# Kernel tuning notes

Measured on AMD Instinct MI355X. Metric: run time of the kernel, lower is better.

The kernel has to match this reference:

```python
import jax, jax.numpy as jnp
import numpy as np

IN_FF = 7  # joints
MASK = np.ones(9, dtype=np.float32)  # [P(3), RPY sin/cos (6)]


def _mlp(x, params):
    # params: list of (W, b); sigmoid after every layer except the last (predict)
    h = x
    for W, b in params[:-1]:
        h = jax.nn.sigmoid(h @ W + b)
    W, b = params[-1]
    return h @ W + b


def _rpy_head(x, params):
    # FeedForwardNet_RPY forward: y -> [sin(y0), cos(y1)], angle = atan2(sin, cos)
    y = _mlp(x, params)
    s = jnp.sin(y[..., 0])
    c = jnp.cos(y[..., 1])
    ang = jnp.arctan2(s, c)
    return jnp.stack([s, c, ang], axis=-1)  # (..., 3)


def setup_inputs():
    key = jax.random.key(0)
    ks = jax.random.split(key, 26)
    m = 16384
    d = {"x": jax.random.normal(ks[0], (m, 2 * IN_FF), jnp.float32)}

    def lin(k, fi, fo, name, i):
        k1, k2 = jax.random.split(k)
        lim = 1.0 / np.sqrt(fi)  # torch Linear default init
        d[name + "_W" + str(i)] = jax.random.uniform(k1, (fi, fo), jnp.float32, -lim, lim)
        d[name + "_b" + str(i)] = jax.random.uniform(k2, (fo,), jnp.float32, -lim, lim)

    idx = 1
    for name, dims in [("pos", [7, 512, 512, 3]), ("roll", [7, 256, 256, 2]),
                       ("pitch", [7, 256, 256, 2]), ("yaw", [7, 256, 256, 2])]:
        for i in range(3):
            lin(ks[idx], dims[i], dims[i + 1], name, i)
            idx += 1
    return d


def _forward(x, pos_p, roll_p, pitch_p, yaw_p):
    mask = jnp.asarray(MASK)
    M_P, M_RPY = mask[:3], mask[3:]
    q, qdot = x[:, :IN_FF], x[:, IN_FF:]

    # position net: forward + per-sample Jacobian (exact, replaces the autograd loop)
    P = _mlp(q, pos_p)                                          # (m, 3)
    J_P = jax.vmap(jax.jacfwd(lambda z: _mlp(z, pos_p)))(q)     # (m, 3, 7)
    vel = jnp.einsum("moi,mi->mo", J_P, qdot)                   # bmm(J_P, jointVels)
    P = P * M_P
    vel = vel * M_P

    heads = []
    for p in (roll_p, pitch_p, yaw_p):
        f = lambda z, p=p: _rpy_head(z, p)
        y = f(q)                                # (m, 3): [sin, cos, angle]
        J = jax.vmap(jax.jacfwd(f))(q)          # (m, 3, 7)
        v = jnp.einsum("moi,mi->mo", J[:, :2, :], qdot)  # (m, 2)
        heads.append((y, J, v))
    (yR, JR, vR), (yPi, JPi, vPi), (yY, JY, vY) = heads

    # order: [roll_sin, pitch_sin, yaw_sin, roll_cos, pitch_cos, yaw_cos]
    RPY = jnp.stack([yR[:, 0], yPi[:, 0], yY[:, 0], yR[:, 1], yPi[:, 1], yY[:, 1]], axis=1) * M_RPY
    vel_RPY = jnp.stack([vR[:, 0], vPi[:, 0], vY[:, 0], vR[:, 1], vPi[:, 1], vY[:, 1]], axis=1) * M_RPY
    J_RPY = jnp.stack([JR[:, 0], JPi[:, 0], JY[:, 0], JR[:, 1], JPi[:, 1], JY[:, 1]], axis=1)  # (m,6,7)

    out = jnp.concatenate([P, RPY, vel, vel_RPY], axis=1)            # (m, 18)
    J_tot = jnp.concatenate([J_P, J_RPY], axis=1)                    # (m, 9, 7)
    out_angles = jnp.concatenate([P, yR[:, 2:3], yPi[:, 2:3], yY[:, 2:3]], axis=1)       # (m, 6)
    J_tot_angles = jnp.concatenate([J_P, JR[:, 2:3], JPi[:, 2:3], JY[:, 2:3]], axis=1)   # (m, 6, 7)
    return out, J_tot, out_angles, J_tot_angles


def reference(x, pos_W0, pos_b0, pos_W1, pos_b1, pos_W2, pos_b2,
              roll_W0, roll_b0, roll_W1, roll_b1, roll_W2, roll_b2,
              pitch_W0, pitch_b0, pitch_W1, pitch_b1, pitch_W2, pitch_b2,
              yaw_W0, yaw_b0, yaw_W1, yaw_b1, yaw_W2, yaw_b2):
    pos_p = [(pos_W0, pos_b0), (pos_W1, pos_b1), (pos_W2, pos_b2)]
    roll_p = [(roll_W0, roll_b0), (roll_W1, roll_b1), (roll_W2, roll_b2)]
    pitch_p = [(pitch_W0, pitch_b0), (pitch_W1, pitch_b1), (pitch_W2, pitch_b2)]
    yaw_p = [(yaw_W0, yaw_b0), (yaw_W1, yaw_b1), (yaw_W2, yaw_b2)]
    return _forward(x, pos_p, roll_p, pitch_p, yaw_p)
```

## Files before the change

### kernel.cpp

```cpp
#include <hip/hip_runtime.h>
#include <math.h>

typedef __attribute__((ext_vector_type(8))) short short8;
typedef __attribute__((ext_vector_type(4))) float floatx4;
typedef __attribute__((ext_vector_type(2))) unsigned uint2v;

__device__ __forceinline__ float sig(float z) { return 1.0f / (1.0f + __expf(-z)); }

__device__ __forceinline__ unsigned short f2bf(float f) {
    unsigned u = __float_as_uint(f);
    u = (u + 0x7FFFu + ((u >> 16) & 1u)) >> 16;
    return (unsigned short)u;
}

__device__ __forceinline__ unsigned cvtpk_bf16(float lo, float hi) {
    unsigned r;
    asm("v_cvt_pk_bf16_f32 %0, %1, %2" : "=v"(r) : "v"(lo), "v"(hi));
    return r;
}

__device__ __forceinline__ void st_pack4(unsigned short* p, float v0, float v1, float v2, float v3) {
    uint2v u;
    u.x = cvtpk_bf16(v0, v1);
    u.y = cvtpk_bf16(v2, v3);
    *(uint2v*)p = u;
}

__global__ void convert_all(const float* __restrict__ s0, const float* __restrict__ s1,
                            const float* __restrict__ s2, const float* __restrict__ s3,
                            unsigned short* __restrict__ ws) {
    int idx = blockIdx.x * 256 + threadIdx.x;
    const float* src; unsigned short* dst; int H, logH, local;
    if (idx < 262144) { src = s0; dst = ws; H = 512; logH = 9; local = idx; }
    else {
        int r = idx - 262144; int m = r >> 16; local = r & 65535;
        H = 256; logH = 8;
        src = (m == 0) ? s1 : (m == 1) ? s2 : s3;
        dst = ws + 262144 + m * 65536;
    }
    int n = local & (H - 1), k = local >> logH;
    int KT = H >> 5;
    int blk = (n >> 4) * KT + (k >> 5);
    int lane = ((k >> 3) & 3) * 16 + (n & 15);
    int j = k & 7;
    dst[(blk * 64 + lane) * 8 + j] = f2bf(src[local]);
}

struct PosS {
    float B0[512], B1[512], W2[1536];
    float Q[4][8], Qd[4][8];
    float Sum[32][3];
};
struct RpyS {
    float B0[256], B1[256], W2[512];
    float Q[8][8], Qd[8][8];
    float Sum[64][2];
};

__global__ __launch_bounds__(256, 3)
void fused_mfma(const float* __restrict__ x,
                const float* __restrict__ pW0, const float* __restrict__ pb0,
                const float* __restrict__ pb1,
                const float* __restrict__ pW2, const float* __restrict__ pb2,
                const float* __restrict__ rW0_, const float* __restrict__ rb0_,
                const float* __restrict__ rb1_,
                const float* __restrict__ rW2_, const float* __restrict__ rb2_,
                const float* __restrict__ piW0, const float* __restrict__ pib0,
                const float* __restrict__ pib1,
                const float* __restrict__ piW2, const float* __restrict__ pib2,
                const float* __restrict__ yW0, const float* __restrict__ yb0,
                const float* __restrict__ yb1,
                const float* __restrict__ yW2, const float* __restrict__ yb2,
                const unsigned short* __restrict__ wsBase,
                float* __restrict__ out, int ns)
{
    extern __shared__ unsigned short sA[];
    __shared__ union { PosS p; RpyS r; } sU;

    const int tid = threadIdx.x;
    const int xcd  = blockIdx.x & 7;
    const int slot = blockIdx.x >> 3;
    const int o_l  = slot / 5, r5 = slot % 5;
    const int o = xcd + (o_l << 3);

    const size_t JTOT = (size_t)ns * 18, OUTA = (size_t)ns * 81, JANG = (size_t)ns * 87;
    const floatx4 z4 = {0.f, 0.f, 0.f, 0.f};
    const int w = tid >> 6, lane = tid & 63;
    const int quad = lane >> 4, col = lane & 15;
    const int srcl = lane & 47;
    const int lxk = lane ^ (quad << 1);

    if (r5 < 2) {
        const int m0 = (o * 2 + r5) * 4;
        const unsigned short* wsW1 = wsBase;

        for (int i = tid; i < 512;  i += 256) { sU.p.B0[i] = pb0[i]; sU.p.B1[i] = pb1[i]; }
        for (int i = tid; i < 1536; i += 256) sU.p.W2[i] = pW2[i];
        if (tid < 56) {
            int m = tid / 14, c = tid % 14;
            float v = x[(m0 + m) * 14 + c];
            if (c < 7) sU.p.Q[m][c] = v; else sU.p.Qd[m][c - 7] = v;
        }
        __syncthreads();

        const float4* W04 = (const float4*)pW0;

        floatx4 acc[2][8];
        #pragma unroll
        for (int rt = 0; rt < 2; rt++)
            #pragma unroll
            for (int ct = 0; ct < 8; ct++) acc[rt][ct] = z4;

        const short8* bbase = (const short8*)wsW1 + (size_t)(w * 8 * 16) * 64 + lane;
        short8 b0[4], b1[4], b2[4];

#define PLD(B, KT) { \
            B[0] = bbase[((cp4 + 0) * 16 + hh8 + (KT)) * 64]; \
            B[1] = bbase[((cp4 + 1) * 16 + hh8 + (KT)) * 64]; \
            B[2] = bbase[((cp4 + 2) * 16 + hh8 + (KT)) * 64]; \
            B[3] = bbase[((cp4 + 3) * 16 + hh8 + (KT)) * 64]; }
#define PST(B, KT) { \
            const short8 a0 = *(const short8*)&sA[(0 * 8 + (KT)) * 512 + (lxk ^ (KT)) * 8]; \
            const short8 a1 = *(const short8*)&sA[(1 * 8 + (KT)) * 512 + (lxk ^ (KT)) * 8]; \
            acc[0][cp4 + 0] = __builtin_amdgcn_mfma_f32_16x16x32_bf16(a0, B[0], acc[0][cp4 + 0], 0, 0, 0); \
            acc[1][cp4 + 0] = __builtin_amdgcn_mfma_f32_16x16x32_bf16(a1, B[0], acc[1][cp4 + 0], 0, 0, 0); \
            acc[0][cp4 + 1] = __builtin_amdgcn_mfma_f32_16x16x32_bf16(a0, B[1], acc[0][cp4 + 1], 0, 0, 0); \
            acc[1][cp4 + 1] = __builtin_amdgcn_mfma_f32_16x16x32_bf16(a1, B[1], acc[1][cp4 + 1], 0, 0, 0); \
            acc[0][cp4 + 2] = __builtin_amdgcn_mfma_f32_16x16x32_bf16(a0, B[2], acc[0][cp4 + 2], 0, 0, 0); \
            acc[1][cp4 + 2] = __builtin_amdgcn_mfma_f32_16x16x32_bf16(a1, B[2], acc[1][cp4 + 2], 0, 0, 0); \
            acc[0][cp4 + 3] = __builtin_amdgcn_mfma_f32_16x16x32_bf16(a0, B[3], acc[0][cp4 + 3], 0, 0, 0); \
            acc[1][cp4 + 3] = __builtin_amdgcn_mfma_f32_16x16x32_bf16(a1, B[3], acc[1][cp4 + 3], 0, 0, 0); }

        #pragma unroll
        for (int hh = 0; hh < 2; ++hh) {
            const int hh8 = hh * 8;
            b0[0] = bbase[(0 * 16 + hh8) * 64];
            b0[1] = bbase[(1 * 16 + hh8) * 64];
            b0[2] = bbase[(2 * 16 + hh8) * 64];
            b0[3] = bbase[(3 * 16 + hh8) * 64];
            {
                const int jh = tid & 1, item = tid >> 1;
                const int s = item >> 5, k8l = item & 31, k8 = (hh << 5) | k8l;
                float q[7], w0v[7][4];
                #pragma unroll
                for (int i = 0; i < 7; i++) {
                    q[i] = sU.p.Q[s][i];
                    float4 a = W04[i * 128 + k8 * 2 + jh];
                    w0v[i][0] = a.x; w0v[i][1] = a.y; w0v[i][2] = a.z; w0v[i][3] = a.w;
                }
                float hv[4], dv[4];
                #pragma unroll
                for (int jj = 0; jj < 4; jj++) {
                    float z = sU.p.B0[k8 * 8 + jh * 4 + jj];
                    #pragma unroll
                    for (int i = 0; i < 7; i++) z = fmaf(q[i], w0v[i][jj], z);
                    float h = sig(z);
                    hv[jj] = h; dv[jj] = h - h * h;
                }
                const int ktl = k8l >> 2, kq = k8l & 3;
                const int kxr = (kq << 4) ^ (kq << 1) ^ ktl;
                const int rr0 = s * 8;
                st_pack4(&sA[((rr0 >> 4) * 8 + ktl) * 512 + (kxr ^ (rr0 & 15)) * 8 + jh * 4],
                         hv[0], hv[1], hv[2], hv[3]);
                #pragma unroll
                for (int i = 0; i < 7; i++) {
                    const int rr = rr0 + 1 + i;
                    st_pack4(&sA[((rr >> 4) * 8 + ktl) * 512 + (kxr ^ (rr & 15)) * 8 + jh * 4],
                             dv[0] * w0v[i][0], dv[1] * w0v[i][1], dv[2] * w0v[i][2], dv[3] * w0v[i][3]);
                }
            }
            __syncthreads();

            #pragma unroll
            for (int cp = 0; cp < 2; ++cp) {
                const int cp4 = cp * 4;
                if (cp) PLD(b0, 0);
                PLD(b1, 1); PLD(b2, 2);
                __builtin_amdgcn_s_setprio(1);
                PST(b0, 0); PLD(b0, 3);
                PST(b1, 1); PLD(b1, 4);
                PST(b2, 2); PLD(b2, 5);
                PST(b0, 3); PLD(b0, 6);
                PST(b1, 4); PLD(b1, 7);
                PST(b2, 5);
                PST(b0, 6);
                PST(b1, 7);
                __builtin_amdgcn_s_setprio(0);
            }
            if (hh == 0) __syncthreads();
        }
#undef PLD
#undef PST

        float ep[2][4][3];
        #pragma unroll
        for (int a = 0; a < 2; a++) for (int b = 0; b < 4; b++) for (int c = 0; c < 3; c++) ep[a][b][c] = 0.f;

        #pragma unroll
        for (int ct = 0; ct < 8; ++ct) {
            const int n = w * 128 + ct * 16 + col;
            const float b1n = sU.p.B1[n];
            const float w20 = sU.p.W2[n * 3], w21 = sU.p.W2[n * 3 + 1], w22 = sU.p.W2[n * 3 + 2];
            #pragma unroll
            for (int rt = 0; rt < 2; ++rt) {
                float z2c = __shfl(acc[rt][ct][0], srcl);
                float h2 = sig(z2c + b1n);
                float d2 = h2 - h2 * h2;
                #pragma unroll
                for (int r = 0; r < 4; ++r) {
                    float gg = ((quad & 1) == 0 && r == 0) ? h2 : d2 * acc[rt][ct][r];
                    ep[rt][r][0] = fmaf(gg, w20, ep[rt][r][0]);
                    ep[rt][r][1] = fmaf(gg, w21, ep[rt][r][1]);
                    ep[rt][r][2] = fmaf(gg, w22, ep[rt][r][2]);
                }
            }
        }

        __syncthreads();
        {
            float* pl = (float*)sA;
            #pragma unroll
            for (int rt = 0; rt < 2; ++rt)
                #pragma unroll
                for (int r = 0; r < 4; ++r) {
                    int row = rt * 16 + quad * 4 + r;
                    int base = ((w * 32 + row) * 3) * 17 + col;
                    pl[base]      = ep[rt][r][0];
                    pl[base + 17] = ep[rt][r][1];
                    pl[base + 34] = ep[rt][r][2];
                }
        }
        __syncthreads();

        if (tid < 96) {
            const float* pl = (const float*)sA;
            int row = tid / 3, j = tid % 3;
            float v = 0.f;
            #pragma unroll
            for (int ww = 0; ww < 4; ++ww) {
                const float* q = &pl[((ww * 32 + row) * 3 + j) * 17];
                #pragma unroll
                for (int c = 0; c < 16; ++c) v += q[c];
            }
            int s = row >> 3, i = row & 7;
            size_t M = m0 + s;
            if (i == 0) { v += pb2[j]; out[M * 18 + j] = v; out[OUTA + M * 6 + j] = v; }
            else        { out[JTOT + M * 63 + j * 7 + (i - 1)] = v;
                          out[JANG + M * 42 + j * 7 + (i - 1)] = v; }
            sU.p.Sum[row][j] = v;
        }
        __syncthreads();
        if (tid < 12) {
            int s = tid / 3, j = tid % 3;
            float vel = 0.f;
            #pragma unroll
            for (int i = 0; i < 7; i++) vel = fmaf(sU.p.Sum[s * 8 + 1 + i][j], sU.p.Qd[s][i], vel);
            out[(size_t)(m0 + s) * 18 + 9 + j] = vel;
        }
    } else {
        const int h = r5 - 2;
        const int m0 = o * 8;
        const float* W0 = (h == 0) ? rW0_ : (h == 1) ? piW0 : yW0;
        const float* b0p = (h == 0) ? rb0_ : (h == 1) ? pib0 : yb0;
        const float* b1p = (h == 0) ? rb1_ : (h == 1) ? pib1 : yb1;
        const float* W2 = (h == 0) ? rW2_ : (h == 1) ? piW2 : yW2;
        const float* b2p = (h == 0) ? rb2_ : (h == 1) ? pib2 : yb2;
        const unsigned short* wsW1 = wsBase + 262144 + h * 65536;

        if (tid < 256) { sU.r.B0[tid] = b0p[tid]; sU.r.B1[tid] = b1p[tid]; }
        for (int i = tid; i < 512; i += 256) sU.r.W2[i] = W2[i];
        if (tid < 112) {
            int m = tid / 14, c = tid % 14;
            float v = x[(m0 + m) * 14 + c];
            if (c < 7) sU.r.Q[m][c] = v; else sU.r.Qd[m][c - 7] = v;
        }
        __syncthreads();

        const float4* W04 = (const float4*)W0;

        floatx4 acc[4][4];
        #pragma unroll
        for (int rt = 0; rt < 4; rt++)
            #pragma unroll
            for (int ct = 0; ct < 4; ct++) acc[rt][ct] = z4;

        const short8* bbase = (const short8*)wsW1 + (size_t)(w * 4 * 8) * 64 + lane;
        short8 b0[2], b1[2], b2[2];

#define RLD(B, KT) { \
            B[0] = bbase[((cp2 + 0) * 8 + hh4 + (KT)) * 64]; \
            B[1] = bbase[((cp2 + 1) * 8 + hh4 + (KT)) * 64]; }
#define RST(B, KT) { \
            const int sw_ = hh4 + (KT); \
            const short8 a0 = *(const short8*)&sA[(0 * 4 + (KT)) * 512 + (lxk ^ sw_) * 8]; \
            const short8 a1 = *(const short8*)&sA[(1 * 4 + (KT)) * 512 + (lxk ^ sw_) * 8]; \
            const short8 a2 = *(const short8*)&sA[(2 * 4 + (KT)) * 512 + (lxk ^ sw_) * 8]; \
            const short8 a3 = *(const short8*)&sA[(3 * 4 + (KT)) * 512 + (lxk ^ sw_) * 8]; \
            acc[0][cp2 + 0] = __builtin_amdgcn_mfma_f32_16x16x32_bf16(a0, B[0], acc[0][cp2 + 0], 0, 0, 0); \
            acc[1][cp2 + 0] = __builtin_amdgcn_mfma_f32_16x16x32_bf16(a1, B[0], acc[1][cp2 + 0], 0, 0, 0); \
            acc[2][cp2 + 0] = __builtin_amdgcn_mfma_f32_16x16x32_bf16(a2, B[0], acc[2][cp2 + 0], 0, 0, 0); \
            acc[3][cp2 + 0] = __builtin_amdgcn_mfma_f32_16x16x32_bf16(a3, B[0], acc[3][cp2 + 0], 0, 0, 0); \
            acc[0][cp2 + 1] = __builtin_amdgcn_mfma_f32_16x16x32_bf16(a0, B[1], acc[0][cp2 + 1], 0, 0, 0); \
            acc[1][cp2 + 1] = __builtin_amdgcn_mfma_f32_16x16x32_bf16(a1, B[1], acc[1][cp2 + 1], 0, 0, 0); \
            acc[2][cp2 + 1] = __builtin_amdgcn_mfma_f32_16x16x32_bf16(a2, B[1], acc[2][cp2 + 1], 0, 0, 0); \
            acc[3][cp2 + 1] = __builtin_amdgcn_mfma_f32_16x16x32_bf16(a3, B[1], acc[3][cp2 + 1], 0, 0, 0); }

        #pragma unroll
        for (int hh = 0; hh < 2; ++hh) {
            const int hh4 = hh * 4;
            b0[0] = bbase[(0 * 8 + hh4) * 64];
            b0[1] = bbase[(1 * 8 + hh4) * 64];
            {
                const int jh = tid & 1, item = tid >> 1;
                const int s = item >> 4, k8l = item & 15, k8 = (hh << 4) | k8l;
                float q[7], w0v[7][4];
                #pragma unroll
                for (int i = 0; i < 7; i++) {
                    q[i] = sU.r.Q[s][i];
                    float4 a = W04[i * 64 + k8 * 2 + jh];
                    w0v[i][0] = a.x; w0v[i][1] = a.y; w0v[i][2] = a.z; w0v[i][3] = a.w;
                }
                float hv[4], dv[4];
                #pragma unroll
                for (int jj = 0; jj < 4; jj++) {
                    float z = sU.r.B0[k8 * 8 + jh * 4 + jj];
                    #pragma unroll
                    for (int i = 0; i < 7; i++) z = fmaf(q[i], w0v[i][jj], z);
                    float hhh = sig(z);
                    hv[jj] = hhh; dv[jj] = hhh - hhh * hhh;
                }
                const int ktl = k8l >> 2, kq = k8l & 3;
                const int sw = (hh << 2) | ktl;
                const int kxr = (kq << 4) ^ (kq << 1) ^ sw;
                const int rr0 = s * 8;
                st_pack4(&sA[((rr0 >> 4) * 4 + ktl) * 512 + (kxr ^ (rr0 & 15)) * 8 + jh * 4],
                         hv[0], hv[1], hv[2], hv[3]);
                #pragma unroll
                for (int i = 0; i < 7; i++) {
                    const int rr = rr0 + 1 + i;
                    st_pack4(&sA[((rr >> 4) * 4 + ktl) * 512 + (kxr ^ (rr & 15)) * 8 + jh * 4],
                             dv[0] * w0v[i][0], dv[1] * w0v[i][1], dv[2] * w0v[i][2], dv[3] * w0v[i][3]);
                }
            }
            __syncthreads();

            #pragma unroll
            for (int cp = 0; cp < 2; ++cp) {
                const int cp2 = cp * 2;
                if (cp) RLD(b0, 0);
                RLD(b1, 1); RLD(b2, 2);
                __builtin_amdgcn_s_setprio(1);
                RST(b0, 0); RLD(b0, 3);
                RST(b1, 1);
                RST(b2, 2);
                RST(b0, 3);
                __builtin_amdgcn_s_setprio(0);
            }
            if (hh == 0) __syncthreads();
        }
#undef RLD
#undef RST

        float ep[4][4][2];
        #pragma unroll
        for (int a = 0; a < 4; a++) for (int b = 0; b < 4; b++) for (int c = 0; c < 2; c++) ep[a][b][c] = 0.f;

        #pragma unroll
        for (int ct = 0; ct < 4; ++ct) {
            const int n = w * 64 + ct * 16 + col;
            const float b1n = sU.r.B1[n];
            const float w20 = sU.r.W2[n * 2], w21 = sU.r.W2[n * 2 + 1];
            #pragma unroll
            for (int rt = 0; rt < 4; ++rt) {
                float z2c = __shfl(acc[rt][ct][0], srcl);
                float h2 = sig(z2c + b1n);
                float d2 = h2 - h2 * h2;
                #pragma unroll
                for (int r = 0; r < 4; ++r) {
                    float gg = ((quad & 1) == 0 && r == 0) ? h2 : d2 * acc[rt][ct][r];
                    ep[rt][r][0] = fmaf(gg, w20, ep[rt][r][0]);
                    ep[rt][r][1] = fmaf(gg, w21, ep[rt][r][1]);
                }
            }
        }

        __syncthreads();
        {
            float* pl = (float*)sA;
            #pragma unroll
            for (int rt = 0; rt < 4; ++rt)
                #pragma unroll
                for (int r = 0; r < 4; ++r) {
                    int row = rt * 16 + quad * 4 + r;
                    int base = ((w * 64 + row) * 2) * 17 + col;
                    pl[base]      = ep[rt][r][0];
                    pl[base + 17] = ep[rt][r][1];
                }
        }
        __syncthreads();

        if (tid < 128) {
            const float* pl = (const float*)sA;
            int row = tid >> 1, j = tid & 1;
            float v = 0.f;
            #pragma unroll
            for (int ww = 0; ww < 4; ++ww) {
                const float* q = &pl[((ww * 64 + row) * 2 + j) * 17];
                #pragma unroll
                for (int c = 0; c < 16; ++c) v += q[c];
            }
            if ((row & 7) == 0) v += b2p[j];
            sU.r.Sum[row][j] = v;
        }
        __syncthreads();

        if (tid < 8) {
            int s = tid;
            size_t M = m0 + s;
            float y0 = sU.r.Sum[s * 8][0], y1 = sU.r.Sum[s * 8][1];
            float sv = sinf(y0), cv = cosf(y1);
            out[M * 18 + 3 + h] = sv;
            out[M * 18 + 6 + h] = cv;
            out[OUTA + M * 6 + 3 + h] = atan2f(sv, cv);
            float f0 = cosf(y0), f1 = -sinf(y1);
            float inv = 1.0f / fmaf(sv, sv, cv * cv);
            float v0 = 0.f, v1 = 0.f;
            #pragma unroll
            for (int i = 0; i < 7; i++) {
                float r0 = f0 * sU.r.Sum[s * 8 + 1 + i][0];
                float r1 = f1 * sU.r.Sum[s * 8 + 1 + i][1];
                out[JTOT + M * 63 + (3 + h) * 7 + i] = r0;
                out[JTOT + M * 63 + (6 + h) * 7 + i] = r1;
                out[JANG + M * 42 + (3 + h) * 7 + i] = (cv * r0 - sv * r1) * inv;
                v0 = fmaf(r0, sU.r.Qd[s][i], v0);
                v1 = fmaf(r1, sU.r.Qd[s][i], v1);
            }
            out[M * 18 + 12 + h] = v0;
            out[M * 18 + 15 + h] = v1;
        }
    }
}

extern "C" void kernel_launch(void* const* d_in, const int* in_sizes, int n_in,
                              void* d_out, int out_size, void* d_ws, size_t ws_size,
                              hipStream_t stream) {
    (void)n_in; (void)out_size; (void)ws_size;
    const float* x = (const float*)d_in[0];
    float* out = (float*)d_out;
    unsigned short* ws = (unsigned short*)d_ws;
    const int ns = in_sizes[0] / 14;

    convert_all<<<dim3(1792), 256, 0, stream>>>(
        (const float*)d_in[3], (const float*)d_in[9],
        (const float*)d_in[15], (const float*)d_in[21], ws);

    fused_mfma<<<dim3((ns / 8) * 5), 256, 34816, stream>>>(
        x,
        (const float*)d_in[1],  (const float*)d_in[2],  (const float*)d_in[4],
        (const float*)d_in[5],  (const float*)d_in[6],
        (const float*)d_in[7],  (const float*)d_in[8],  (const float*)d_in[10],
        (const float*)d_in[11], (const float*)d_in[12],
        (const float*)d_in[13], (const float*)d_in[14], (const float*)d_in[16],
        (const float*)d_in[17], (const float*)d_in[18],
        (const float*)d_in[19], (const float*)d_in[20], (const float*)d_in[22],
        (const float*)d_in[23], (const float*)d_in[24],
        ws, out, ns);
}
```

Measured before the change: 288.5 us.

## Build full layer-1 activation tile once instead of two K halves

The layer-0 activation/Jacobian tile for the full K dimension is now written to shared memory in a single pass, and layer 1 runs as one continuous MFMA loop over all K tiles. This removes the second build phase and its barriers, and gives the B-operand prefetch pipeline a longer steady state. B1 and W2 are loaded into registers early and stored to shared memory after the MFMA loop, so they reuse the freed space and the pre-epilogue barrier is dropped. In exchange the shared-memory footprint for the A tile doubles, which may lower occupancy, and more registers stay live across the loop.

```diff
diff --git a/kernel.cpp b/kernel.cpp
--- a/kernel.cpp
+++ b/kernel.cpp
@@ -94,8 +94,12 @@
         const int m0 = (o * 2 + r5) * 4;
         const unsigned short* wsW1 = wsBase;
 
-        for (int i = tid; i < 512;  i += 256) { sU.p.B0[i] = pb0[i]; sU.p.B1[i] = pb1[i]; }
-        for (int i = tid; i < 1536; i += 256) sU.p.W2[i] = pW2[i];
+        const float b1r0 = pb1[tid], b1r1 = pb1[tid + 256];
+        float w2r[6];
+        #pragma unroll
+        for (int t = 0; t < 6; ++t) w2r[t] = pW2[tid + 256 * t];
+
+        for (int i = tid; i < 512; i += 256) sU.p.B0[i] = pb0[i];
         if (tid < 56) {
             int m = tid / 14, c = tid % 14;
             float v = x[(m0 + m) * 14 + c];
@@ -115,13 +119,14 @@
         short8 b0[4], b1[4], b2[4];
 
 #define PLD(B, KT) { \
-            B[0] = bbase[((cp4 + 0) * 16 + hh8 + (KT)) * 64]; \
-            B[1] = bbase[((cp4 + 1) * 16 + hh8 + (KT)) * 64]; \
-            B[2] = bbase[((cp4 + 2) * 16 + hh8 + (KT)) * 64]; \
-            B[3] = bbase[((cp4 + 3) * 16 + hh8 + (KT)) * 64]; }
+            B[0] = bbase[((cp4 + 0) * 16 + (KT)) * 64]; \
+            B[1] = bbase[((cp4 + 1) * 16 + (KT)) * 64]; \
+            B[2] = bbase[((cp4 + 2) * 16 + (KT)) * 64]; \
+            B[3] = bbase[((cp4 + 3) * 16 + (KT)) * 64]; }
 #define PST(B, KT) { \
-            const short8 a0 = *(const short8*)&sA[(0 * 8 + (KT)) * 512 + (lxk ^ (KT)) * 8]; \
-            const short8 a1 = *(const short8*)&sA[(1 * 8 + (KT)) * 512 + (lxk ^ (KT)) * 8]; \
+            const int sw_ = (KT) & 7; \
+            const short8 a0 = *(const short8*)&sA[(0 * 16 + (KT)) * 512 + (lxk ^ sw_) * 8]; \
+            const short8 a1 = *(const short8*)&sA[(1 * 16 + (KT)) * 512 + (lxk ^ sw_) * 8]; \
             acc[0][cp4 + 0] = __builtin_amdgcn_mfma_f32_16x16x32_bf16(a0, B[0], acc[0][cp4 + 0], 0, 0, 0); \
             acc[1][cp4 + 0] = __builtin_amdgcn_mfma_f32_16x16x32_bf16(a1, B[0], acc[1][cp4 + 0], 0, 0, 0); \
             acc[0][cp4 + 1] = __builtin_amdgcn_mfma_f32_16x16x32_bf16(a0, B[1], acc[0][cp4 + 1], 0, 0, 0); \
@@ -131,66 +136,77 @@
             acc[0][cp4 + 3] = __builtin_amdgcn_mfma_f32_16x16x32_bf16(a0, B[3], acc[0][cp4 + 3], 0, 0, 0); \
             acc[1][cp4 + 3] = __builtin_amdgcn_mfma_f32_16x16x32_bf16(a1, B[3], acc[1][cp4 + 3], 0, 0, 0); }
 
-        #pragma unroll
-        for (int hh = 0; hh < 2; ++hh) {
-            const int hh8 = hh * 8;
-            b0[0] = bbase[(0 * 16 + hh8) * 64];
-            b0[1] = bbase[(1 * 16 + hh8) * 64];
-            b0[2] = bbase[(2 * 16 + hh8) * 64];
-            b0[3] = bbase[(3 * 16 + hh8) * 64];
-            {
-                const int jh = tid & 1, item = tid >> 1;
-                const int s = item >> 5, k8l = item & 31, k8 = (hh << 5) | k8l;
-                float q[7], w0v[7][4];
-                #pragma unroll
-                for (int i = 0; i < 7; i++) {
-                    q[i] = sU.p.Q[s][i];
-                    float4 a = W04[i * 128 + k8 * 2 + jh];
-                    w0v[i][0] = a.x; w0v[i][1] = a.y; w0v[i][2] = a.z; w0v[i][3] = a.w;
-                }
-                float hv[4], dv[4];
-                #pragma unroll
-                for (int jj = 0; jj < 4; jj++) {
-                    float z = sU.p.B0[k8 * 8 + jh * 4 + jj];
-                    #pragma unroll
-                    for (int i = 0; i < 7; i++) z = fmaf(q[i], w0v[i][jj], z);
-                    float h = sig(z);
-                    hv[jj] = h; dv[jj] = h - h * h;
-                }
-                const int ktl = k8l >> 2, kq = k8l & 3;
-                const int kxr = (kq << 4) ^ (kq << 1) ^ ktl;
-                const int rr0 = s * 8;
-                st_pack4(&sA[((rr0 >> 4) * 8 + ktl) * 512 + (kxr ^ (rr0 & 15)) * 8 + jh * 4],
-                         hv[0], hv[1], hv[2], hv[3]);
-                #pragma unroll
-                for (int i = 0; i < 7; i++) {
-                    const int rr = rr0 + 1 + i;
-                    st_pack4(&sA[((rr >> 4) * 8 + ktl) * 512 + (kxr ^ (rr & 15)) * 8 + jh * 4],
-                             dv[0] * w0v[i][0], dv[1] * w0v[i][1], dv[2] * w0v[i][2], dv[3] * w0v[i][3]);
-                }
-            }
-            __syncthreads();
-
-            #pragma unroll
-            for (int cp = 0; cp < 2; ++cp) {
-                const int cp4 = cp * 4;
-                if (cp) PLD(b0, 0);
-                PLD(b1, 1); PLD(b2, 2);
-                __builtin_amdgcn_s_setprio(1);
-                PST(b0, 0); PLD(b0, 3);
-                PST(b1, 1); PLD(b1, 4);
-                PST(b2, 2); PLD(b2, 5);
-                PST(b0, 3); PLD(b0, 6);
-                PST(b1, 4); PLD(b1, 7);
-                PST(b2, 5);
-                PST(b0, 6);
-                PST(b1, 7);
-                __builtin_amdgcn_s_setprio(0);
-            }
-            if (hh == 0) __syncthreads();
+        {
+            const int cp4 = 0;
+            PLD(b0, 0);
+        }
+
+        #pragma unroll
+        for (int t = 0; t < 2; ++t) {
+            const int item = tid + t * 256;
+            const int jh = item & 1, it2 = item >> 1;
+            const int s = it2 >> 6, k8 = it2 & 63;
+            float q[7], w0v[7][4];
+            #pragma unroll
+            for (int i = 0; i < 7; i++) {
+                q[i] = sU.p.Q[s][i];
+                float4 a = W04[i * 128 + k8 * 2 + jh];
+                w0v[i][0] = a.x; w0v[i][1] = a.y; w0v[i][2] = a.z; w0v[i][3] = a.w;
+            }
+            float hv[4], dv[4];
+            #pragma unroll
+            for (int jj = 0; jj < 4; jj++) {
+                float z = sU.p.B0[k8 * 8 + jh * 4 + jj];
+                #pragma unroll
+                for (int i = 0; i < 7; i++) z = fmaf(q[i], w0v[i][jj], z);
+                float h = sig(z);
+                hv[jj] = h; dv[jj] = h - h * h;
+            }
+            const int ktg = k8 >> 2, kq = k8 & 3;
+            const int kxr = (kq << 4) ^ (kq << 1) ^ (ktg & 7);
+            const int rr0 = s * 8;
+            st_pack4(&sA[((rr0 >> 4) * 16 + ktg) * 512 + (kxr ^ (rr0 & 15)) * 8 + jh * 4],
+                     hv[0], hv[1], hv[2], hv[3]);
+            #pragma unroll
+            for (int i = 0; i < 7; i++) {
+                const int rr = rr0 + 1 + i;
+                st_pack4(&sA[((rr >> 4) * 16 + ktg) * 512 + (kxr ^ (rr & 15)) * 8 + jh * 4],
+                         dv[0] * w0v[i][0], dv[1] * w0v[i][1], dv[2] * w0v[i][2], dv[3] * w0v[i][3]);
+            }
+        }
+        __syncthreads();
+
+        #pragma unroll
+        for (int cp = 0; cp < 2; ++cp) {
+            const int cp4 = cp * 4;
+            if (cp) PLD(b0, 0);
+            PLD(b1, 1); PLD(b2, 2);
+            __builtin_amdgcn_s_setprio(1);
+            PST(b0, 0);  PLD(b0, 3);
+            PST(b1, 1);  PLD(b1, 4);
+            PST(b2, 2);  PLD(b2, 5);
+            PST(b0, 3);  PLD(b0, 6);
+            PST(b1, 4);  PLD(b1, 7);
+            PST(b2, 5);  PLD(b2, 8);
+            PST(b0, 6);  PLD(b0, 9);
+            PST(b1, 7);  PLD(b1, 10);
+            PST(b2, 8);  PLD(b2, 11);
+            PST(b0, 9);  PLD(b0, 12);
+            PST(b1, 10); PLD(b1, 13);
+            PST(b2, 11); PLD(b2, 14);
+            PST(b0, 12); PLD(b0, 15);
+            PST(b1, 13);
+            PST(b2, 14);
+            PST(b0, 15);
+            __builtin_amdgcn_s_setprio(0);
         }
 #undef PLD
 #undef PST
+
+        sU.p.B1[tid] = b1r0; sU.p.B1[tid + 256] = b1r1;
+        #pragma unroll
+        for (int t = 0; t < 6; ++t) sU.p.W2[tid + 256 * t] = w2r[t];
+        __syncthreads();
 
         float ep[2][4][3];
         #pragma unroll
@@ -216,7 +232,6 @@
             }
         }
 
-        __syncthreads();
         {
             float* pl = (float*)sA;
             #pragma unroll
@@ -267,8 +282,10 @@
         const float* b2p = (h == 0) ? rb2_ : (h == 1) ? pib2 : yb2;
         const unsigned short* wsW1 = wsBase + 262144 + h * 65536;
 
-        if (tid < 256) { sU.r.B0[tid] = b0p[tid]; sU.r.B1[tid] = b1p[tid]; }
-        for (int i = tid; i < 512; i += 256) sU.r.W2[i] = W2[i];
+        const float b1r0 = b1p[tid];
+        const float w2r0 = W2[tid], w2r1 = W2[tid + 256];
+
+        if (tid < 256) sU.r.B0[tid] = b0p[tid];
         if (tid < 112) {
             int m = tid / 14, c = tid % 14;
             float v = x[(m0 + m) * 14 + c];
@@ -288,14 +305,13 @@
         short8 b0[2], b1[2], b2[2];
 
 #define RLD(B, KT) { \
-            B[0] = bbase[((cp2 + 0) * 8 + hh4 + (KT)) * 64]; \
-            B[1] = bbase[((cp2 + 1) * 8 + hh4 + (KT)) * 64]; }
+            B[0] = bbase[((cp2 + 0) * 8 + (KT)) * 64]; \
+            B[1] = bbase[((cp2 + 1) * 8 + (KT)) * 64]; }
 #define RST(B, KT) { \
-            const int sw_ = hh4 + (KT); \
-            const short8 a0 = *(const short8*)&sA[(0 * 4 + (KT)) * 512 + (lxk ^ sw_) * 8]; \
-            const short8 a1 = *(const short8*)&sA[(1 * 4 + (KT)) * 512 + (lxk ^ sw_) * 8]; \
-            const short8 a2 = *(const short8*)&sA[(2 * 4 + (KT)) * 512 + (lxk ^ sw_) * 8]; \
-            const short8 a3 = *(const short8*)&sA[(3 * 4 + (KT)) * 512 + (lxk ^ sw_) * 8]; \
+            const short8 a0 = *(const short8*)&sA[(0 * 8 + (KT)) * 512 + (lxk ^ (KT)) * 8]; \
+            const short8 a1 = *(const short8*)&sA[(1 * 8 + (KT)) * 512 + (lxk ^ (KT)) * 8]; \
+            const short8 a2 = *(const short8*)&sA[(2 * 8 + (KT)) * 512 + (lxk ^ (KT)) * 8]; \
+            const short8 a3 = *(const short8*)&sA[(3 * 8 + (KT)) * 512 + (lxk ^ (KT)) * 8]; \
             acc[0][cp2 + 0] = __builtin_amdgcn_mfma_f32_16x16x32_bf16(a0, B[0], acc[0][cp2 + 0], 0, 0, 0); \
             acc[1][cp2 + 0] = __builtin_amdgcn_mfma_f32_16x16x32_bf16(a1, B[0], acc[1][cp2 + 0], 0, 0, 0); \
             acc[2][cp2 + 0] = __builtin_amdgcn_mfma_f32_16x16x32_bf16(a2, B[0], acc[2][cp2 + 0], 0, 0, 0); \
@@ -305,61 +321,68 @@
             acc[2][cp2 + 1] = __builtin_amdgcn_mfma_f32_16x16x32_bf16(a2, B[1], acc[2][cp2 + 1], 0, 0, 0); \
             acc[3][cp2 + 1] = __builtin_amdgcn_mfma_f32_16x16x32_bf16(a3, B[1], acc[3][cp2 + 1], 0, 0, 0); }
 
-        #pragma unroll
-        for (int hh = 0; hh < 2; ++hh) {
-            const int hh4 = hh * 4;
-            b0[0] = bbase[(0 * 8 + hh4) * 64];
-            b0[1] = bbase[(1 * 8 + hh4) * 64];
-            {
-                const int jh = tid & 1, item = tid >> 1;
-                const int s = item >> 4, k8l = item & 15, k8 = (hh << 4) | k8l;
-                float q[7], w0v[7][4];
-                #pragma unroll
-                for (int i = 0; i < 7; i++) {
-                    q[i] = sU.r.Q[s][i];
-                    float4 a = W04[i * 64 + k8 * 2 + jh];
-                    w0v[i][0] = a.x; w0v[i][1] = a.y; w0v[i][2] = a.z; w0v[i][3] = a.w;
-                }
-                float hv[4], dv[4];
-                #pragma unroll
-                for (int jj = 0; jj < 4; jj++) {
-                    float z = sU.r.B0[k8 * 8 + jh * 4 + jj];
-                    #pragma unroll
-                    for (int i = 0; i < 7; i++) z = fmaf(q[i], w0v[i][jj], z);
-                    float hhh = sig(z);
-                    hv[jj] = hhh; dv[jj] = hhh - hhh * hhh;
-                }
-                const int ktl = k8l >> 2, kq = k8l & 3;
-                const int sw = (hh << 2) | ktl;
-                const int kxr = (kq << 4) ^ (kq << 1) ^ sw;
-                const int rr0 = s * 8;
-                st_pack4(&sA[((rr0 >> 4) * 4 + ktl) * 512 + (kxr ^ (rr0 & 15)) * 8 + jh * 4],
-                         hv[0], hv[1], hv[2], hv[3]);
-                #pragma unroll
-                for (int i = 0; i < 7; i++) {
-                    const int rr = rr0 + 1 + i;
-                    st_pack4(&sA[((rr >> 4) * 4 + ktl) * 512 + (kxr ^ (rr & 15)) * 8 + jh * 4],
-                             dv[0] * w0v[i][0], dv[1] * w0v[i][1], dv[2] * w0v[i][2], dv[3] * w0v[i][3]);
-                }
-            }
-            __syncthreads();
-
-            #pragma unroll
-            for (int cp = 0; cp < 2; ++cp) {
-                const int cp2 = cp * 2;
-                if (cp) RLD(b0, 0);
-                RLD(b1, 1); RLD(b2, 2);
-                __builtin_amdgcn_s_setprio(1);
-                RST(b0, 0); RLD(b0, 3);
-                RST(b1, 1);
-                RST(b2, 2);
-                RST(b0, 3);
-                __builtin_amdgcn_s_setprio(0);
-            }
-            if (hh == 0) __syncthreads();
+        {
+            const int cp2 = 0;
+            RLD(b0, 0);
+        }
+
+        #pragma unroll
+        for (int t = 0; t < 2; ++t) {
+            const int item = tid + t * 256;
+            const int jh = item & 1, it2 = item >> 1;
+            const int s = it2 >> 5, k8 = it2 & 31;
+            float q[7], w0v[7][4];
+            #pragma unroll
+            for (int i = 0; i < 7; i++) {
+                q[i] = sU.r.Q[s][i];
+                float4 a = W04[i * 64 + k8 * 2 + jh];
+                w0v[i][0] = a.x; w0v[i][1] = a.y; w0v[i][2] = a.z; w0v[i][3] = a.w;
+            }
+            float hv[4], dv[4];
+            #pragma unroll
+            for (int jj = 0; jj < 4; jj++) {
+                float z = sU.r.B0[k8 * 8 + jh * 4 + jj];
+                #pragma unroll
+                for (int i = 0; i < 7; i++) z = fmaf(q[i], w0v[i][jj], z);
+                float hhh = sig(z);
+                hv[jj] = hhh; dv[jj] = hhh - hhh * hhh;
+            }
+            const int ktg = k8 >> 2, kq = k8 & 3;
+            const int kxr = (kq << 4) ^ (kq << 1) ^ ktg;
+            const int rr0 = s * 8;
+            st_pack4(&sA[((rr0 >> 4) * 8 + ktg) * 512 + (kxr ^ (rr0 & 15)) * 8 + jh * 4],
+                     hv[0], hv[1], hv[2], hv[3]);
+            #pragma unroll
+            for (int i = 0; i < 7; i++) {
+                const int rr = rr0 + 1 + i;
+                st_pack4(&sA[((rr >> 4) * 8 + ktg) * 512 + (kxr ^ (rr & 15)) * 8 + jh * 4],
+                         dv[0] * w0v[i][0], dv[1] * w0v[i][1], dv[2] * w0v[i][2], dv[3] * w0v[i][3]);
+            }
+        }
+        __syncthreads();
+
+        #pragma unroll
+        for (int cp = 0; cp < 2; ++cp) {
+            const int cp2 = cp * 2;
+            if (cp) RLD(b0, 0);
+            RLD(b1, 1); RLD(b2, 2);
+            __builtin_amdgcn_s_setprio(1);
+            RST(b0, 0); RLD(b0, 3);
+            RST(b1, 1); RLD(b1, 4);
+            RST(b2, 2); RLD(b2, 5);
+            RST(b0, 3); RLD(b0, 6);
+            RST(b1, 4); RLD(b1, 7);
+            RST(b2, 5);
+            RST(b0, 6);
+            RST(b1, 7);
+            __builtin_amdgcn_s_setprio(0);
         }
 #undef RLD
 #undef RST
+
+        sU.r.B1[tid] = b1r0;
+        sU.r.W2[tid] = w2r0; sU.r.W2[tid + 256] = w2r1;
+        __syncthreads();
 
         float ep[4][4][2];
         #pragma unroll
@@ -384,7 +407,6 @@
             }
         }
 
-        __syncthreads();
         {
             float* pl = (float*)sA;
             #pragma unroll
```

New measurement: 286.9 us. Within noise of the previous version (-0.6%).
